# Kernel tuning notes

Measured on AMD Instinct MI355X. Metric: run time of the kernel, lower is better.

The kernel has to match this reference:

```python
import math
import jax, jax.numpy as jnp
import numpy as np

TWO_PI = 2.0 * math.pi

def ring_pe(s, K):
    # s: [N] in [0,1). Returns [N, 2K]: interleaved cos/sin harmonics k=1..K.
    k = jnp.arange(1, K + 1, dtype=s.dtype)            # [K]
    ang = TWO_PI * s[:, None] * k[None, :]             # [N, K]
    pe = jnp.stack([jnp.cos(ang), jnp.sin(ang)], axis=-1)  # [N, K, 2]
    return pe.reshape(s.shape[0], 2 * K)

def setup_inputs() -> dict:
    key = jax.random.key(0)
    k1, k2, k3, k4 = jax.random.split(key, 4)
    N, Z, H, K = 2048, 32, 64, 2
    in_dim = 2 * (2 * K) + 2 + Z  # 42
    return {
        "z_g": jax.random.normal(k1, (1, Z), dtype=jnp.float32),
        "s": jax.random.uniform(k2, (N,), dtype=jnp.float32),
        "W1": jax.random.normal(k3, (in_dim, H), dtype=jnp.float32) * (1.0 / math.sqrt(in_dim)),
        "b1": jnp.zeros((H,), dtype=jnp.float32),
        "W2": jax.random.normal(k4, (H, 1), dtype=jnp.float32) * (1.0 / math.sqrt(H)),
        "b2": jnp.zeros((1,), dtype=jnp.float32),
        "K": K,
    }

def reference(z_g, s, W1, b1, W2, b2, K):
    N = s.shape[0]
    pe = ring_pe(s, K)                                  # [N, 2K]
    pe_i = jnp.broadcast_to(pe[:, None, :], (N, N, pe.shape[-1]))
    pe_j = jnp.broadcast_to(pe[None, :, :], (N, N, pe.shape[-1]))
    diff = s[:, None] - s[None, :]
    diff = diff - jnp.floor(diff)
    diff = jnp.minimum(diff, 1.0 - diff)                # circular distance in [0, 0.5]
    diff_pe = jnp.stack([jnp.cos(TWO_PI * diff), jnp.sin(TWO_PI * diff)], axis=-1)  # [N, N, 2]
    zrep = jnp.broadcast_to(z_g.reshape(1, 1, -1), (N, N, z_g.shape[-1]))
    x = jnp.concatenate([pe_i, pe_j, diff_pe, zrep], axis=-1)  # [N, N, 42]
    h = jax.nn.relu(jnp.einsum('ijd,dh->ijh', x, W1) + b1)
    logits = (jnp.einsum('ijh,ho->ijo', h, W2) + b2)[..., 0]   # [N, N]
    logits = 0.5 * (logits + logits.T)
    eye = jnp.eye(N, dtype=bool)
    return jnp.where(eye, jnp.float32(-1e9), logits)
```

## Files before the change

kernel.cpp:

```cpp
#include <hip/hip_runtime.h>
#include <math.h>

#define TWO_PI_F 6.28318530717958647692f

typedef unsigned int u32;
typedef __attribute__((ext_vector_type(4))) float    f4;
typedef __attribute__((ext_vector_type(16))) float   f16v;
typedef __attribute__((ext_vector_type(2))) float    f2;
typedef __attribute__((ext_vector_type(2))) _Float16 h2;
typedef __attribute__((ext_vector_type(4))) _Float16 h4;
typedef __attribute__((ext_vector_type(8))) _Float16 h8;

union B8 { h8 v; h4 q[2]; };

#if __has_builtin(__builtin_amdgcn_fdot2)
#define FDOT2(a, b, c) __builtin_amdgcn_fdot2((a), (b), (c), false)
#else
__device__ __forceinline__ float FDOT2(h2 a, h2 b, float c) {
    return c + (float)a[0] * (float)b[0] + (float)a[1] * (float)b[1];
}
#endif

#if __has_builtin(__builtin_amdgcn_cvt_pkrtz)
__device__ __forceinline__ h2 CVTPK(float a, float b) {
    return __builtin_bit_cast(h2, __builtin_amdgcn_cvt_pkrtz(a, b));
}
#else
__device__ __forceinline__ h2 CVTPK(float a, float b) {
    return (h2){(_Float16)a, (_Float16)b};
}
#endif

__global__ __launch_bounds__(256, 4) void gd_mfma(
    const float* __restrict__ z,  const float* __restrict__ s,
    const float* __restrict__ W1, const float* __restrict__ b1,
    const float* __restrict__ W2, const float* __restrict__ b2v,
    float* __restrict__ out, int N, int NB)
{
    __shared__ __attribute__((aligned(16))) _Float16 Ald[64][24];
    __shared__ __attribute__((aligned(16))) h4 peb[64];
    __shared__ __attribute__((aligned(16))) h4 P2[1024];
    __shared__ __attribute__((aligned(16))) h2 w2p[32];
    __shared__ __attribute__((aligned(16))) float S[2][32][36];
    __shared__ f2 strig[64];
    __shared__ h4 zq;

    int u = blockIdx.x;
    int M = 2 * NB + 1;
    float disc = (float)(M * M - 8 * u);
    int bi = (int)(((float)M - sqrtf(disc)) * 0.5f);
    if (bi < 0) bi = 0;
    if (bi > NB - 1) bi = NB - 1;
    while (bi > 0 && bi * (M - bi) / 2 > u) --bi;
    while ((bi + 1) * (M - (bi + 1)) / 2 <= u) ++bi;
    int bj = bi + (u - bi * (M - bi) / 2);

    int t    = threadIdx.x;
    int lane = t & 63;

    if (t == 0) zq = (h4)0;
    if (t >= 64 && t < 96) {
        int r2 = t - 64;
        w2p[r2] = (h2){(_Float16)(0.5f * W2[2 * r2]),
                       (_Float16)(0.5f * W2[2 * r2 + 1])};
    }
    if (t < 64) {
        int grow = (t < 32) ? (bi * 32 + t) : (bj * 32 + (t - 32));
        float ang = TWO_PI_F * s[grow];
        float c1 = __cosf(ang), s1 = __sinf(ang);
        float c2 = c1 * c1 - s1 * s1, s2 = 2.0f * c1 * s1;
        strig[t] = (f2){c1, s1};
        peb[t]   = (h4){(_Float16)c1, (_Float16)s1, (_Float16)c2, (_Float16)s2};

        float zc = b1[t];
#pragma unroll
        for (int zz = 0; zz < 32; ++zz)
            zc = fmaf(z[zz], W1[(10 + zz) * 64 + t], zc);

        h8 row0, row1;
#pragma unroll
        for (int k = 0; k < 8; ++k) row0[k] = (_Float16)W1[k * 64 + t];
        row1 = (h8)0;
        row1[0] = (_Float16)W1[8 * 64 + t];
        row1[1] = (_Float16)W1[9 * 64 + t];
        row1[2] = (_Float16)zc;
        *(h8*)&Ald[t][0] = row0;
        *(h8*)&Ald[t][8] = row1;
    }
    __syncthreads();

    {
        int base = t * 4;
        int il = base >> 5, j0 = base & 31;
        f2 ci = strig[il];
#pragma unroll
        for (int c = 0; c < 4; ++c) {
            f2 cj = strig[32 + j0 + c];
            float ctv = fmaf(ci.x, cj.x, ci.y * cj.y);
            float stv = fabsf(fmaf(ci.y, cj.x, -(ci.x * cj.y)));
            P2[base + c] = (h4){(_Float16)ctv, (_Float16)stv,
                                (_Float16)1.0f, (_Float16)0.0f};
        }
    }

    int n = lane & 31;
    int q = lane >> 5;

    h8 afr[2];
    h2 w2h[2][8];
#pragma unroll
    for (int H = 0; H < 2; ++H) {
        afr[H] = *(const h8*)&Ald[H * 32 + n][q * 8];
#pragma unroll
        for (int e = 0; e < 8; ++e)
            w2h[H][e] = w2p[(e & 1) + 4 * (e >> 1) + 2 * q + 16 * H];
    }
    __syncthreads();

    int wv = t >> 6;
#pragma unroll 4
    for (int i = 0; i < 16; ++i) {
        int g  = wv * 16 + i;
        int o  = g >> 5;
        int il = g & 31;
        int cell = il * 32 + n;

        int rA = o ? (32 + n) : il;
        int rB = o ? il : (32 + n);
        const h4* pa = q ? &P2[cell] : &peb[rA];
        const h4* pb = q ? &zq : &peb[rB];

        B8 bfr;
        bfr.q[0] = *pa;
        bfr.q[1] = *pb;

        f16v a0 = __builtin_amdgcn_mfma_f32_32x32x16_f16(afr[0], bfr.v, (f16v)(0.0f), 0, 0, 0);
        f16v a1 = __builtin_amdgcn_mfma_f32_32x32x16_f16(afr[1], bfr.v, (f16v)(0.0f), 0, 0, 0);

        float ps = 0.0f;
#pragma unroll
        for (int e = 0; e < 8; ++e) {
            h2 m0 = __builtin_elementwise_max(CVTPK(a0[2 * e], a0[2 * e + 1]), (h2)0);
            ps = FDOT2(m0, w2h[0][e], ps);
            h2 m1 = __builtin_elementwise_max(CVTPK(a1[2 * e], a1[2 * e + 1]), (h2)0);
            ps = FDOT2(m1, w2h[1][e], ps);
        }
        ps += __shfl_xor(ps, 32);
        if (q == 0) S[o][il][n] = ps;
    }
    __syncthreads();

    float b2 = b2v[0];
    {
        int il = t >> 3;
        int j0 = (t & 7) * 4;
        f4 a = *(const f4*)&S[0][il][j0];
        f4 b = *(const f4*)&S[1][il][j0];
        f4 v;
#pragma unroll
        for (int c = 0; c < 4; ++c) {
            float x = a[c] + b[c] + b2;
            if (bi == bj && il == j0 + c) x = -1e9f;
            v[c] = x;
        }
        *(f4*)&out[(size_t)(bi * 32 + il) * N + bj * 32 + j0] = v;

        if (bj > bi) {
            int jl = t >> 3;
            int i0 = (t & 7) * 4;
            f4 m;
#pragma unroll
            for (int c = 0; c < 4; ++c)
                m[c] = S[0][i0 + c][jl] + S[1][i0 + c][jl] + b2;
            *(f4*)&out[(size_t)(bj * 32 + jl) * N + bi * 32 + i0] = m;
        }
    }
}

extern "C" void kernel_launch(void* const* d_in, const int* in_sizes, int n_in,
                              void* d_out, int out_size, void* d_ws, size_t ws_size,
                              hipStream_t stream) {
    const float* z  = (const float*)d_in[0];
    const float* s  = (const float*)d_in[1];
    const float* W1 = (const float*)d_in[2];
    const float* b1 = (const float*)d_in[3];
    const float* W2 = (const float*)d_in[4];
    const float* b2 = (const float*)d_in[5];
    int N = in_sizes[1];

    float* out = (float*)d_out;
    int NB = N / 32;
    int nblk = NB * (NB + 1) / 2;
    gd_mfma<<<nblk, 256, 0, stream>>>(z, s, W1, b1, W2, b2, out, N, NB);
}
```

Baseline: 29.05 us.

## Process two rows per iteration with split accumulators and compact pair table

The main loop now gives each wave a fixed orientation and half of the rows. Each iteration issues four independent MFMAs for two rows, and the FDOT2 reduction is split across four accumulators per row. This shortens dependency chains and lets MFMA latency overlap with the epilogue math. The pair trig table shrinks from h4 to h2, with the constant 1.0 and zero lanes built in registers, and the zero-quad shared slot is removed. Holding more live accumulators raises register pressure, which may hurt occupancy at the 4-blocks launch bound.

```diff
diff --git a/kernel.cpp b/kernel.cpp
--- a/kernel.cpp
+++ b/kernel.cpp
@@ -12,6 +12,8 @@
 typedef __attribute__((ext_vector_type(8))) _Float16 h8;
 
 union B8 { h8 v; h4 q[2]; };
+union C2 { u32 w[2]; h4 v; };
+union P4 { h2 a[4]; h8 v; };
 
 #if __has_builtin(__builtin_amdgcn_fdot2)
 #define FDOT2(a, b, c) __builtin_amdgcn_fdot2((a), (b), (c), false)
@@ -39,11 +41,10 @@
 {
     __shared__ __attribute__((aligned(16))) _Float16 Ald[64][24];
     __shared__ __attribute__((aligned(16))) h4 peb[64];
-    __shared__ __attribute__((aligned(16))) h4 P2[1024];
+    __shared__ __attribute__((aligned(16))) h2 P2[1024];
     __shared__ __attribute__((aligned(16))) h2 w2p[32];
     __shared__ __attribute__((aligned(16))) float S[2][32][36];
     __shared__ f2 strig[64];
-    __shared__ h4 zq;
 
     int u = blockIdx.x;
     int M = 2 * NB + 1;
@@ -58,7 +59,6 @@
     int t    = threadIdx.x;
     int lane = t & 63;
 
-    if (t == 0) zq = (h4)0;
     if (t >= 64 && t < 96) {
         int r2 = t - 64;
         w2p[r2] = (h2){(_Float16)(0.5f * W2[2 * r2]),
@@ -93,14 +93,15 @@
         int base = t * 4;
         int il = base >> 5, j0 = base & 31;
         f2 ci = strig[il];
+        P4 pk;
 #pragma unroll
         for (int c = 0; c < 4; ++c) {
             f2 cj = strig[32 + j0 + c];
             float ctv = fmaf(ci.x, cj.x, ci.y * cj.y);
             float stv = fabsf(fmaf(ci.y, cj.x, -(ci.x * cj.y)));
-            P2[base + c] = (h4){(_Float16)ctv, (_Float16)stv,
-                                (_Float16)1.0f, (_Float16)0.0f};
-        }
+            pk.a[c] = CVTPK(ctv, stv);
+        }
+        *(h8*)&P2[base] = pk.v;
     }
 
     int n = lane & 31;
@@ -117,36 +118,71 @@
     }
     __syncthreads();
 
-    int wv = t >> 6;
-#pragma unroll 4
-    for (int i = 0; i < 16; ++i) {
-        int g  = wv * 16 + i;
-        int o  = g >> 5;
-        int il = g & 31;
-        int cell = il * 32 + n;
-
-        int rA = o ? (32 + n) : il;
-        int rB = o ? il : (32 + n);
-        const h4* pa = q ? &P2[cell] : &peb[rA];
-        const h4* pb = q ? &zq : &peb[rB];
-
-        B8 bfr;
-        bfr.q[0] = *pa;
-        bfr.q[1] = *pb;
-
-        f16v a0 = __builtin_amdgcn_mfma_f32_32x32x16_f16(afr[0], bfr.v, (f16v)(0.0f), 0, 0, 0);
-        f16v a1 = __builtin_amdgcn_mfma_f32_32x32x16_f16(afr[1], bfr.v, (f16v)(0.0f), 0, 0, 0);
-
-        float ps = 0.0f;
+    int wv   = t >> 6;
+    int o    = wv >> 1;
+    int base = (wv & 1) * 16;
+
+    h4 pe_inv = peb[32 + n];
+
+#pragma unroll
+    for (int i = 0; i < 8; ++i) {
+        int ilA = base + i;
+        int ilB = base + i + 8;
+
+        h4 varA = peb[ilA];
+        h4 varB = peb[ilB];
+        u32 pwA = *(const u32*)&P2[ilA * 32 + n];
+        u32 pwB = *(const u32*)&P2[ilB * 32 + n];
+
+        B8 bA, bB;
+        {
+            h4 pa = o ? pe_inv : varA;
+            h4 pb = o ? varA : pe_inv;
+            C2 cc; cc.w[0] = pwA; cc.w[1] = 0x00003C00u;
+            bA.q[0] = q ? cc.v : pa;
+            bA.q[1] = q ? (h4)0 : pb;
+        }
+        {
+            h4 pa = o ? pe_inv : varB;
+            h4 pb = o ? varB : pe_inv;
+            C2 cc; cc.w[0] = pwB; cc.w[1] = 0x00003C00u;
+            bB.q[0] = q ? cc.v : pa;
+            bB.q[1] = q ? (h4)0 : pb;
+        }
+
+        f16v a0A = __builtin_amdgcn_mfma_f32_32x32x16_f16(afr[0], bA.v, (f16v)(0.0f), 0, 0, 0);
+        f16v a1A = __builtin_amdgcn_mfma_f32_32x32x16_f16(afr[1], bA.v, (f16v)(0.0f), 0, 0, 0);
+        f16v a0B = __builtin_amdgcn_mfma_f32_32x32x16_f16(afr[0], bB.v, (f16v)(0.0f), 0, 0, 0);
+        f16v a1B = __builtin_amdgcn_mfma_f32_32x32x16_f16(afr[1], bB.v, (f16v)(0.0f), 0, 0, 0);
+
+        float pA0 = 0.f, pA1 = 0.f, pA2 = 0.f, pA3 = 0.f;
+        float pB0 = 0.f, pB1 = 0.f, pB2 = 0.f, pB3 = 0.f;
 #pragma unroll
         for (int e = 0; e < 8; ++e) {
-            h2 m0 = __builtin_elementwise_max(CVTPK(a0[2 * e], a0[2 * e + 1]), (h2)0);
-            ps = FDOT2(m0, w2h[0][e], ps);
-            h2 m1 = __builtin_elementwise_max(CVTPK(a1[2 * e], a1[2 * e + 1]), (h2)0);
-            ps = FDOT2(m1, w2h[1][e], ps);
-        }
-        ps += __shfl_xor(ps, 32);
-        if (q == 0) S[o][il][n] = ps;
+            h2 mA0 = __builtin_elementwise_max(CVTPK(a0A[2 * e], a0A[2 * e + 1]), (h2)0);
+            h2 mA1 = __builtin_elementwise_max(CVTPK(a1A[2 * e], a1A[2 * e + 1]), (h2)0);
+            h2 mB0 = __builtin_elementwise_max(CVTPK(a0B[2 * e], a0B[2 * e + 1]), (h2)0);
+            h2 mB1 = __builtin_elementwise_max(CVTPK(a1B[2 * e], a1B[2 * e + 1]), (h2)0);
+            if (e & 1) {
+                pA1 = FDOT2(mA0, w2h[0][e], pA1);
+                pA3 = FDOT2(mA1, w2h[1][e], pA3);
+                pB1 = FDOT2(mB0, w2h[0][e], pB1);
+                pB3 = FDOT2(mB1, w2h[1][e], pB3);
+            } else {
+                pA0 = FDOT2(mA0, w2h[0][e], pA0);
+                pA2 = FDOT2(mA1, w2h[1][e], pA2);
+                pB0 = FDOT2(mB0, w2h[0][e], pB0);
+                pB2 = FDOT2(mB1, w2h[1][e], pB2);
+            }
+        }
+        float psA = (pA0 + pA1) + (pA2 + pA3);
+        float psB = (pB0 + pB1) + (pB2 + pB3);
+        psA += __shfl_xor(psA, 32);
+        psB += __shfl_xor(psB, 32);
+        if (q == 0) {
+            S[o][ilA][n] = psA;
+            S[o][ilB][n] = psB;
+        }
     }
     __syncthreads();
 
```

Result: no change. 29.01 us (-0.1%).
